# Kernel optimization log

Measured on AMD Instinct MI355X. Metric: run time of the kernel, lower is better.

The kernel has to match this reference:

```python
import jax, jax.numpy as jnp
import numpy as np

FEATURE_DIM = 512
DEPTH = 128
NUM_CLASSES = 1000


def setup_inputs() -> dict:
    key = jax.random.key(0)
    ks = jax.random.split(key, 9)
    s = 1.0 / np.sqrt(FEATURE_DIM)
    sd = 1.0 / np.sqrt(DEPTH)
    return {
        "x": jax.random.normal(ks[0], (8, 2048, FEATURE_DIM), dtype=jnp.float32),
        "Wq": jax.random.uniform(ks[1], (FEATURE_DIM, DEPTH), jnp.float32, -s, s),
        "bq": jax.random.uniform(ks[2], (DEPTH,), jnp.float32, -s, s),
        "Wk": jax.random.uniform(ks[3], (FEATURE_DIM, DEPTH), jnp.float32, -s, s),
        "bk": jax.random.uniform(ks[4], (DEPTH,), jnp.float32, -s, s),
        "Wv": jax.random.uniform(ks[5], (FEATURE_DIM, DEPTH), jnp.float32, -s, s),
        "bv": jax.random.uniform(ks[6], (DEPTH,), jnp.float32, -s, s),
        "Wl": jax.random.uniform(ks[7], (DEPTH, NUM_CLASSES), jnp.float32, -sd, sd),
        "bl": jax.random.uniform(ks[8], (NUM_CLASSES,), jnp.float32, -sd, sd),
    }


def reference(x, Wq, bq, Wk, bk, Wv, bv, Wl, bl):
    # q,k,v: [B,S,depth]
    q = jnp.einsum("bsf,fd->bsd", x, Wq) + bq
    k = jnp.einsum("bsf,fd->bsd", x, Wk) + bk
    v = jnp.einsum("bsf,fd->bsd", x, Wv) + bv
    # NOTE: original applies no 1/sqrt(depth) scaling
    logit = jnp.einsum("bqd,bkd->bqk", q, k)  # [B,S,S]
    attn = jax.nn.softmax(logit, axis=2)
    attn_out = jnp.einsum("bqk,bkd->bqd", attn, v)  # [B,S,depth]
    out = jnp.einsum("bsd,dc->bsc", attn_out, Wl) + bl  # [B,S,C]
    return out.mean(axis=1)  # [B,C]
```

## Files before the change

### kernel.cpp

```cpp
#include <hip/hip_runtime.h>
#include <stdint.h>

#define NB 8
#define SS 2048
#define FF 512
#define DD 128
#define CC 1000
#define KC 8
#define CHUNK (SS / KC)

typedef __attribute__((ext_vector_type(8))) short bf16x8;
typedef __attribute__((ext_vector_type(4))) float f32x4;

__device__ __forceinline__ short f2bf(float f) {
    uint32_t u;
    __builtin_memcpy(&u, &f, 4);
    u = (u + 0x7fffu + ((u >> 16) & 1u)) >> 16;
    return (short)u;
}
__device__ __forceinline__ float bf2f(short h) {
    uint32_t u = ((uint32_t)(uint16_t)h) << 16;
    float f;
    __builtin_memcpy(&f, &u, 4);
    return f;
}
__device__ __forceinline__ void async16(const void* g, void* l) {
    __builtin_amdgcn_global_load_lds(
        (const __attribute__((address_space(1))) uint32_t*)g,
        (__attribute__((address_space(3))) uint32_t*)l, 16, 0, 0);
}

__global__ void prep(const float* __restrict__ x,
                     const float* __restrict__ Wq, const float* __restrict__ Wk,
                     const float* __restrict__ Wv,
                     short* __restrict__ xb, short* __restrict__ Wt)
{
    int bx = blockIdx.x;
    if (bx < 4096) {
        int id = bx * 256 + threadIdx.x;
        const float4* src = (const float4*)x + id * 2;
        float4 a = src[0], b2 = src[1];
        bf16x8 o;
        o[0] = f2bf(a.x);  o[1] = f2bf(a.y);  o[2] = f2bf(a.z);  o[3] = f2bf(a.w);
        o[4] = f2bf(b2.x); o[5] = f2bf(b2.y); o[6] = f2bf(b2.z); o[7] = f2bf(b2.w);
        *(bf16x8*)(xb + id * 8) = o;
    } else {
        int id = (bx - 4096) * 256 + threadIdx.x;
        int w = id >> 16, rem = id & 65535;
        int n = rem >> 9, kx = rem & 511;
        const float* Wsrc = (w == 0) ? Wq : (w == 1) ? Wk : Wv;
        Wt[w * 65536 + n * 512 + kx] = f2bf(Wsrc[kx * 128 + n]);
    }
}

__global__ __launch_bounds__(256) void qkv_proj(
    const short* __restrict__ xb, const short* __restrict__ Wt,
    const float* __restrict__ bq, const float* __restrict__ bk, const float* __restrict__ bv,
    short* __restrict__ qo, short* __restrict__ ko, short* __restrict__ vo)
{
    __shared__ __align__(16) short As[2][128 * 64];
    __shared__ __align__(16) short Bs[2][128 * 64];

    const int m0   = blockIdx.x * 128;
    const int mat  = blockIdx.y;
    const int tid  = threadIdx.x;
    const int wave = tid >> 6, lane = tid & 63;
    const int quad = lane >> 4, l16 = lane & 15;
    const int wr = wave >> 1, wc = wave & 1;

    const short* Wm = Wt + mat * 65536;

    f32x4 acc[4][4];
    for (int i = 0; i < 4; i++)
        for (int j = 0; j < 4; j++) acc[i][j] = (f32x4){0.f, 0.f, 0.f, 0.f};

    const int sr = lane >> 3;
    const int sc = (lane & 7) ^ (sr & 7);

#define QKV_STAGE(buf, kk)                                                  \
    for (int i = 0; i < 4; i++) {                                           \
        int ins = wave * 4 + i;                                             \
        int r = ins * 8 + sr;                                               \
        async16(xb + (m0 + r) * 512 + (kk) + sc * 8, &As[buf][ins * 512]);  \
        async16(Wm + r * 512 + (kk) + sc * 8,        &Bs[buf][ins * 512]);  \
    }

    QKV_STAGE(0, 0)
    __syncthreads();

    int cur = 0;
    for (int t = 0; t < 8; t++) {
        if (t < 7) { QKV_STAGE(cur ^ 1, (t + 1) * 64) }

        for (int kc = 0; kc < 2; kc++) {
            bf16x8 af[4], bfr[4];
            for (int mt = 0; mt < 4; mt++) {
                int R = wr * 64 + mt * 16 + l16, cc = kc * 4 + quad;
                af[mt] = *(const bf16x8*)&As[cur][(R * 8 + (cc ^ (R & 7))) * 8];
            }
            for (int nt = 0; nt < 4; nt++) {
                int R = wc * 64 + nt * 16 + l16, cc = kc * 4 + quad;
                bfr[nt] = *(const bf16x8*)&Bs[cur][(R * 8 + (cc ^ (R & 7))) * 8];
            }
            for (int mt = 0; mt < 4; mt++)
                for (int nt = 0; nt < 4; nt++)
                    acc[mt][nt] = __builtin_amdgcn_mfma_f32_16x16x32_bf16(
                        af[mt], bfr[nt], acc[mt][nt], 0, 0, 0);
        }
        __syncthreads();
        cur ^= 1;
    }
#undef QKV_STAGE

    const float* bias = (mat == 0) ? bq : (mat == 1) ? bk : bv;
    short* outp = (mat == 0) ? qo : (mat == 1) ? ko : vo;
    for (int mt = 0; mt < 4; mt++) {
        int grow_base = m0 + wr * 64 + mt * 16 + quad * 4;
        for (int nt = 0; nt < 4; nt++) {
            int col = wc * 64 + nt * 16 + l16;
            float bb = bias[col];
            for (int r = 0; r < 4; r++)
                outp[(grow_base + r) * 128 + col] = f2bf(acc[mt][nt][r] + bb);
        }
    }
}

__global__ __launch_bounds__(256) void attn_l(
    const short* __restrict__ q, const short* __restrict__ k,
    float* __restrict__ l_part, float* __restrict__ accum)
{
    __shared__ __align__(16) short ks[2][64 * 128];

    const int b  = blockIdx.y;
    const int q0 = blockIdx.x * 128;
    const int lq = blockIdx.z;
    const int c0 = lq * CHUNK;
    const int tid  = threadIdx.x;
    const int wave = tid >> 6, lane = tid & 63;
    const int quad = lane >> 4, l16 = lane & 15;

    if (blockIdx.x == 0 && blockIdx.y == 0 && blockIdx.z == 0) {
        accum[tid] = 0.f; accum[256 + tid] = 0.f;
        accum[512 + tid] = 0.f; accum[768 + tid] = 0.f;
    }

    bf16x8 qf[2][4];
    for (int m = 0; m < 2; m++)
        for (int c = 0; c < 4; c++)
            qf[m][c] = *(const bf16x8*)(q + (b * 2048 + q0 + wave * 32 + m * 16 + l16) * 128
                                          + c * 32 + quad * 8);

    float lsum[2][4] = {{0.f,0.f,0.f,0.f},{0.f,0.f,0.f,0.f}};
    const int krl = lane >> 4;

#define K_STAGE(buf, s0)                                                     \
    for (int i = 0; i < 4; i++) {                                            \
        int ik = wave * 4 + i;                                               \
        int kr = ik * 4 + krl;                                               \
        int kc8 = (lane & 15) ^ (kr & 15);                                   \
        async16(k + (b * 2048 + (s0) + kr) * 128 + kc8 * 8, &ks[buf][ik * 512]); \
    }

    K_STAGE(0, c0)
    __syncthreads();

    int cur = 0;
    for (int t = 0; t < CHUNK / 64; t++) {
        if (t < CHUNK / 64 - 1) { K_STAGE(cur ^ 1, c0 + (t + 1) * 64) }

        for (int ct = 0; ct < 4; ct++) {
            f32x4 Sf[2];
            Sf[0] = (f32x4){0.f,0.f,0.f,0.f};
            Sf[1] = (f32x4){0.f,0.f,0.f,0.f};
            int R = ct * 16 + l16;
            __builtin_amdgcn_s_setprio(1);
            for (int c = 0; c < 4; c++) {
                int cc = c * 4 + quad;
                bf16x8 kb = *(const bf16x8*)&ks[cur][(R * 16 + (cc ^ l16)) * 8];
                for (int m = 0; m < 2; m++)
                    Sf[m] = __builtin_amdgcn_mfma_f32_16x16x32_bf16(
                        qf[m][c], kb, Sf[m], 0, 0, 0);
            }
            __builtin_amdgcn_s_setprio(0);
            for (int m = 0; m < 2; m++)
                for (int r = 0; r < 4; r++)
                    lsum[m][r] += __expf(Sf[m][r] - 10.0f);
        }
        __syncthreads();
        cur ^= 1;
    }

    for (int m = 0; m < 2; m++)
        for (int r = 0; r < 4; r++) {
            float lv = lsum[m][r];
            lv += __shfl_xor(lv, 1);
            lv += __shfl_xor(lv, 2);
            lv += __shfl_xor(lv, 4);
            lv += __shfl_xor(lv, 8);
            if (l16 == 0)
                l_part[(lq * 8 + b) * 2048 + q0 + wave * 32 + m * 16 + quad * 4 + r] = lv;
        }
}

__global__ __launch_bounds__(256) void attn_w(
    const short* __restrict__ q, const short* __restrict__ k,
    const float* __restrict__ l_part, float* __restrict__ w_part)
{
    __shared__ __align__(16) short ks[2][64 * 128];
    __shared__ float wl[4][256];

    const int b  = blockIdx.y;
    const int qt = blockIdx.x;
    const int q0 = qt * 128;
    const int lq = blockIdx.z;
    const int c0 = lq * CHUNK;
    const int tid  = threadIdx.x;
    const int wave = tid >> 6, lane = tid & 63;
    const int quad = lane >> 4, l16 = lane & 15;

    bf16x8 qf[2][4];
    for (int m = 0; m < 2; m++)
        for (int c = 0; c < 4; c++)
            qf[m][c] = *(const bf16x8*)(q + (b * 2048 + q0 + wave * 32 + m * 16 + l16) * 128
                                          + c * 32 + quad * 8);

    float linv[2][4];
    for (int m = 0; m < 2; m++)
        for (int r = 0; r < 4; r++) {
            int row = q0 + wave * 32 + m * 16 + quad * 4 + r;
            float lt = 0.f;
            for (int kc = 0; kc < KC; kc++) lt += l_part[(kc * 8 + b) * 2048 + row];
            linv[m][r] = 1.0f / lt;
        }

    const int krl = lane >> 4;

    K_STAGE(0, c0)
    __syncthreads();

    int cur = 0;
    for (int t = 0; t < CHUNK / 64; t++) {
        if (t < CHUNK / 64 - 1) { K_STAGE(cur ^ 1, c0 + (t + 1) * 64) }
        int s0 = c0 + t * 64;

        for (int ct = 0; ct < 4; ct++) {
            f32x4 Sf[2];
            Sf[0] = (f32x4){0.f,0.f,0.f,0.f};
            Sf[1] = (f32x4){0.f,0.f,0.f,0.f};
            int R = ct * 16 + l16;
            __builtin_amdgcn_s_setprio(1);
            for (int c = 0; c < 4; c++) {
                int cc = c * 4 + quad;
                bf16x8 kb = *(const bf16x8*)&ks[cur][(R * 16 + (cc ^ l16)) * 8];
                for (int m = 0; m < 2; m++)
                    Sf[m] = __builtin_amdgcn_mfma_f32_16x16x32_bf16(
                        qf[m][c], kb, Sf[m], 0, 0, 0);
            }
            __builtin_amdgcn_s_setprio(0);
            float cs = 0.f;
            for (int m = 0; m < 2; m++)
                for (int r = 0; r < 4; r++)
                    cs += __expf(Sf[m][r] - 10.0f) * linv[m][r];
            cs += __shfl_xor(cs, 16);
            cs += __shfl_xor(cs, 32);
            if (quad == 0) wl[wave][(s0 - c0) + ct * 16 + l16] = cs;
        }
        __syncthreads();
        cur ^= 1;
    }
#undef K_STAGE

    {
        float s = wl[0][tid] + wl[1][tid] + wl[2][tid] + wl[3][tid];
        w_part[(qt * 8 + b) * 2048 + c0 + tid] = s;
    }
}

__global__ __launch_bounds__(256) void wv(
    const float* __restrict__ w_part, const short* __restrict__ vo,
    float* __restrict__ accum)
{
    __shared__ float wsh[128];
    __shared__ float red[16][129];
    const int b    = blockIdx.x;
    const int slab = blockIdx.y;
    const int tid  = threadIdx.x;

    if (tid < 128) {
        int s = slab * 128 + tid;
        float wsum = 0.f;
        for (int qt = 0; qt < 16; qt++) wsum += w_part[(qt * 8 + b) * 2048 + s];
        wsh[tid] = wsum;
    }
    __syncthreads();

    const int dgrp = tid & 15, sgrp = tid >> 4;
    const int d0 = dgrp * 8;
    float a[8] = {0.f,0.f,0.f,0.f,0.f,0.f,0.f,0.f};
    for (int i = 0; i < 8; i++) {
        int sl = sgrp * 8 + i;
        bf16x8 v = *(const bf16x8*)(vo + (size_t)(b * 2048 + slab * 128 + sl) * 128 + d0);
        float w = wsh[sl];
        for (int j = 0; j < 8; j++) a[j] += w * bf2f(v[j]);
    }
    for (int j = 0; j < 8; j++) red[sgrp][d0 + j] = a[j];
    __syncthreads();

    if (tid < 128) {
        float s = 0.f;
        for (int g = 0; g < 16; g++) s += red[g][tid];
        atomicAdd(&accum[b * 128 + tid], s);
    }
}

__global__ void final_proj(const float* __restrict__ accum, const float* __restrict__ Wl,
                           const float* __restrict__ bl, float* __restrict__ out)
{
    int id = blockIdx.x * 256 + threadIdx.x;
    if (id >= NB * CC) return;
    int b = id / CC, c = id % CC;
    float s = 0.f;
    for (int d = 0; d < 128; d++)
        s += accum[b * 128 + d] * Wl[d * 1000 + c];
    out[id] = s * (1.0f / 2048.0f) + bl[c];
}

extern "C" void kernel_launch(void* const* d_in, const int* in_sizes, int n_in,
                              void* d_out, int out_size, void* d_ws, size_t ws_size,
                              hipStream_t stream) {
    const float* x  = (const float*)d_in[0];
    const float* Wq = (const float*)d_in[1];
    const float* bq = (const float*)d_in[2];
    const float* Wk = (const float*)d_in[3];
    const float* bk = (const float*)d_in[4];
    const float* Wv = (const float*)d_in[5];
    const float* bv = (const float*)d_in[6];
    const float* Wl = (const float*)d_in[7];
    const float* bl = (const float*)d_in[8];
    float* out = (float*)d_out;

    char* ws = (char*)d_ws;
    short* qo     = (short*)(ws);
    short* ko     = (short*)(ws + 4194304);
    short* vo     = (short*)(ws + 8388608);
    short* xb     = (short*)(ws + 12582912);
    short* Wt     = (short*)(ws + 29360128);
    float* l_part = (float*)(ws + 29753344);
    float* w_part = (float*)(ws + 30277632);
    float* acc    = (float*)(ws + 31326208);

    prep<<<4864, 256, 0, stream>>>(x, Wq, Wk, Wv, xb, Wt);
    qkv_proj<<<dim3(128, 3), 256, 0, stream>>>(xb, Wt, bq, bk, bv, qo, ko, vo);
    attn_l<<<dim3(16, 8, KC), 256, 0, stream>>>(qo, ko, l_part, acc);
    attn_w<<<dim3(16, 8, KC), 256, 0, stream>>>(qo, ko, l_part, w_part);
    wv<<<dim3(8, 16), 256, 0, stream>>>(w_part, vo, acc);
    final_proj<<<(NB * CC + 255) / 256, 256, 0, stream>>>(acc, Wl, bl, out);
}
```

Measured before the change: 148.6 us.

## Store exp scores as bf16 in attn_l and reuse them in attn_wp

In the first attention pass, the exponentiated scores are packed to bf16 and written to a large workspace buffer. A new kernel then reads them back, applies the row normalisation and reduces column weights, so the QK^T MFMA work is not recomputed in a second pass. This replaces recomputation with 64 MB of extra global writes and reads. The buffer overlaps the xb region that prep and qkv_proj no longer need, and it is used only when the workspace is large enough. The stored probabilities are also rounded to bf16, which adds precision loss.

New measurement: 148.8 us. No clear change (+0.1%).

```diff
diff --git a/kernel.cpp b/kernel.cpp
--- a/kernel.cpp
+++ b/kernel.cpp
@@ -11,6 +11,7 @@
 
 typedef __attribute__((ext_vector_type(8))) short bf16x8;
 typedef __attribute__((ext_vector_type(4))) float f32x4;
+typedef __attribute__((ext_vector_type(4))) unsigned int u32x4;
 
 __device__ __forceinline__ short f2bf(float f) {
     uint32_t u;
@@ -23,6 +24,11 @@
     float f;
     __builtin_memcpy(&f, &u, 4);
     return f;
+}
+__device__ __forceinline__ uint32_t cvtpk(float a, float b) {
+    uint32_t r;
+    asm("v_cvt_pk_bf16_f32 %0, %1, %2" : "=v"(r) : "v"(a), "v"(b));
+    return r;
 }
 __device__ __forceinline__ void async16(const void* g, void* l) {
     __builtin_amdgcn_global_load_lds(
@@ -127,19 +133,21 @@
 
 __global__ __launch_bounds__(256) void attn_l(
     const short* __restrict__ q, const short* __restrict__ k,
-    float* __restrict__ l_part, float* __restrict__ accum)
+    float* __restrict__ l_part, float* __restrict__ accum,
+    uint32_t* __restrict__ Pbuf)
 {
     __shared__ __align__(16) short ks[2][64 * 128];
 
     const int b  = blockIdx.y;
-    const int q0 = blockIdx.x * 128;
+    const int qt = blockIdx.x;
+    const int q0 = qt * 128;
     const int lq = blockIdx.z;
     const int c0 = lq * CHUNK;
     const int tid  = threadIdx.x;
     const int wave = tid >> 6, lane = tid & 63;
     const int quad = lane >> 4, l16 = lane & 15;
 
-    if (blockIdx.x == 0 && blockIdx.y == 0 && blockIdx.z == 0) {
+    if (qt == 0 && b == 0 && lq == 0) {
         accum[tid] = 0.f; accum[256 + tid] = 0.f;
         accum[512 + tid] = 0.f; accum[768 + tid] = 0.f;
     }
@@ -152,6 +160,7 @@
 
     float lsum[2][4] = {{0.f,0.f,0.f,0.f},{0.f,0.f,0.f,0.f}};
     const int krl = lane >> 4;
+    const size_t pbase = (size_t)((lq * 8 + b) * 16 + qt) * 16384;
 
 #define K_STAGE(buf, s0)                                                     \
     for (int i = 0; i < 4; i++) {                                            \
@@ -182,9 +191,21 @@
                         qf[m][c], kb, Sf[m], 0, 0, 0);
             }
             __builtin_amdgcn_s_setprio(0);
+            float ev[2][4];
             for (int m = 0; m < 2; m++)
-                for (int r = 0; r < 4; r++)
-                    lsum[m][r] += __expf(Sf[m][r] - 10.0f);
+                for (int r = 0; r < 4; r++) {
+                    ev[m][r] = __expf(Sf[m][r] - 10.0f);
+                    lsum[m][r] += ev[m][r];
+                }
+            if (Pbuf) {
+                u32x4 pk;
+                pk[0] = cvtpk(ev[0][0], ev[0][1]);
+                pk[1] = cvtpk(ev[0][2], ev[0][3]);
+                pk[2] = cvtpk(ev[1][0], ev[1][1]);
+                pk[3] = cvtpk(ev[1][2], ev[1][3]);
+                *(u32x4*)(Pbuf + pbase
+                          + (size_t)((((t * 4 + ct) * 4 + wave) * 64 + lane) * 4)) = pk;
+            }
         }
         __syncthreads();
         cur ^= 1;
@@ -200,6 +221,57 @@
             if (l16 == 0)
                 l_part[(lq * 8 + b) * 2048 + q0 + wave * 32 + m * 16 + quad * 4 + r] = lv;
         }
+}
+
+__global__ __launch_bounds__(256) void attn_wp(
+    const float* __restrict__ l_part, const uint32_t* __restrict__ Pbuf,
+    float* __restrict__ w_part)
+{
+    __shared__ float wl[4][256];
+
+    const int b  = blockIdx.y;
+    const int qt = blockIdx.x;
+    const int q0 = qt * 128;
+    const int lq = blockIdx.z;
+    const int tid  = threadIdx.x;
+    const int wave = tid >> 6, lane = tid & 63;
+    const int quad = lane >> 4, l16 = lane & 15;
+
+    float linv[2][4];
+    for (int m = 0; m < 2; m++)
+        for (int r = 0; r < 4; r++) {
+            int row = q0 + wave * 32 + m * 16 + quad * 4 + r;
+            float lt = 0.f;
+            for (int kc = 0; kc < KC; kc++) lt += l_part[(kc * 8 + b) * 2048 + row];
+            linv[m][r] = 1.0f / lt;
+        }
+
+    const size_t pbase = (size_t)((lq * 8 + b) * 16 + qt) * 16384;
+
+    for (int t = 0; t < CHUNK / 64; t++) {
+        for (int ct = 0; ct < 4; ct++) {
+            u32x4 pk = *(const u32x4*)(Pbuf + pbase
+                        + (size_t)((((t * 4 + ct) * 4 + wave) * 64 + lane) * 4));
+            float cs = 0.f;
+            cs += bf2f((short)(pk[0] & 0xffff)) * linv[0][0];
+            cs += bf2f((short)(pk[0] >> 16))    * linv[0][1];
+            cs += bf2f((short)(pk[1] & 0xffff)) * linv[0][2];
+            cs += bf2f((short)(pk[1] >> 16))    * linv[0][3];
+            cs += bf2f((short)(pk[2] & 0xffff)) * linv[1][0];
+            cs += bf2f((short)(pk[2] >> 16))    * linv[1][1];
+            cs += bf2f((short)(pk[3] & 0xffff)) * linv[1][2];
+            cs += bf2f((short)(pk[3] >> 16))    * linv[1][3];
+            cs += __shfl_xor(cs, 16);
+            cs += __shfl_xor(cs, 32);
+            if (quad == 0) wl[wave][t * 64 + ct * 16 + l16] = cs;
+        }
+    }
+
+    __syncthreads();
+    {
+        float s = wl[0][tid] + wl[1][tid] + wl[2][tid] + wl[3][tid];
+        w_part[(qt * 8 + b) * 2048 + lq * CHUNK + tid] = s;
+    }
 }
 
 __global__ __launch_bounds__(256) void attn_w(
@@ -340,19 +412,39 @@
     float* out = (float*)d_out;
 
     char* ws = (char*)d_ws;
-    short* qo     = (short*)(ws);
-    short* ko     = (short*)(ws + 4194304);
-    short* vo     = (short*)(ws + 8388608);
-    short* xb     = (short*)(ws + 12582912);
-    short* Wt     = (short*)(ws + 29360128);
-    float* l_part = (float*)(ws + 29753344);
-    float* w_part = (float*)(ws + 30277632);
-    float* acc    = (float*)(ws + 31326208);
+    short* qo = (short*)(ws);
+    short* ko = (short*)(ws + 4194304);
+    short* vo = (short*)(ws + 8388608);
+
+    const size_t P_REQ = 81268736ull;
+    bool use_p = ws_size >= P_REQ;
+
+    uint32_t* Pbuf;
+    short *xb, *Wt;
+    float *l_part, *w_part, *acc;
+    if (use_p) {
+        Pbuf   = (uint32_t*)(ws + 12582912);
+        xb     = (short*)(ws + 12582912);
+        Wt     = (short*)(ws + 29360128);
+        l_part = (float*)(ws + 79691776);
+        w_part = (float*)(ws + 80216064);
+        acc    = (float*)(ws + 81264640);
+    } else {
+        Pbuf   = nullptr;
+        xb     = (short*)(ws + 12582912);
+        Wt     = (short*)(ws + 29360128);
+        l_part = (float*)(ws + 29753344);
+        w_part = (float*)(ws + 30277632);
+        acc    = (float*)(ws + 31326208);
+    }
 
     prep<<<4864, 256, 0, stream>>>(x, Wq, Wk, Wv, xb, Wt);
     qkv_proj<<<dim3(128, 3), 256, 0, stream>>>(xb, Wt, bq, bk, bv, qo, ko, vo);
-    attn_l<<<dim3(16, 8, KC), 256, 0, stream>>>(qo, ko, l_part, acc);
-    attn_w<<<dim3(16, 8, KC), 256, 0, stream>>>(qo, ko, l_part, w_part);
+    attn_l<<<dim3(16, 8, KC), 256, 0, stream>>>(qo, ko, l_part, acc, Pbuf);
+    if (use_p)
+        attn_wp<<<dim3(16, 8, KC), 256, 0, stream>>>(l_part, Pbuf, w_part);
+    else
+        attn_w<<<dim3(16, 8, KC), 256, 0, stream>>>(qo, ko, l_part, w_part);
     wv<<<dim3(8, 16), 256, 0, stream>>>(w_part, vo, acc);
     final_proj<<<(NB * CC + 255) / 256, 256, 0, stream>>>(acc, Wl, bl, out);
 }
```

## Fuse attention row-sum and weight passes with grid barrier and register-cached probabilities

Applied to the files above, without the earlier changes.

Merges the two attention kernels into one. The exponentiated scores are kept in registers as packed bf16 and reused after a grid-wide atomic barrier once the row sums are complete, so QK^T no longer has to be recomputed in a second pass. KC drops to 4 so all 512 blocks can be co-resident at two blocks per CU, and q is prescaled by log2(e) so a raw v_exp_f32 replaces __expf. The exchange is high register pressure (128 packed values per thread), bf16 rounding of the probabilities, and a spin barrier that deadlocks if the blocks are not all resident at once.

After: 252.8 us. 70.0% more time.

```diff
diff --git a/kernel.cpp b/kernel.cpp
--- a/kernel.cpp
+++ b/kernel.cpp
@@ -6,8 +6,9 @@
 #define FF 512
 #define DD 128
 #define CC 1000
-#define KC 8
+#define KC 4
 #define CHUNK (SS / KC)
+#define NBLK (16 * 8 * KC)
 
 typedef __attribute__((ext_vector_type(8))) short bf16x8;
 typedef __attribute__((ext_vector_type(4))) float f32x4;
@@ -23,6 +24,16 @@
     float f;
     __builtin_memcpy(&f, &u, 4);
     return f;
+}
+__device__ __forceinline__ uint32_t cvtpk(float a, float b) {
+    uint32_t r;
+    asm("v_cvt_pk_bf16_f32 %0, %1, %2" : "=v"(r) : "v"(a), "v"(b));
+    return r;
+}
+__device__ __forceinline__ float exp2_hw(float x) {
+    float r;
+    asm("v_exp_f32 %0, %1" : "=v"(r) : "v"(x));
+    return r;
 }
 __device__ __forceinline__ void async16(const void* g, void* l) {
     __builtin_amdgcn_global_load_lds(
@@ -56,7 +67,8 @@
 __global__ __launch_bounds__(256) void qkv_proj(
     const short* __restrict__ xb, const short* __restrict__ Wt,
     const float* __restrict__ bq, const float* __restrict__ bk, const float* __restrict__ bv,
-    short* __restrict__ qo, short* __restrict__ ko, short* __restrict__ vo)
+    short* __restrict__ qo, short* __restrict__ ko, short* __restrict__ vo,
+    unsigned int* __restrict__ sem)
 {
     __shared__ __align__(16) short As[2][128 * 64];
     __shared__ __align__(16) short Bs[2][128 * 64];
@@ -68,6 +80,8 @@
     const int quad = lane >> 4, l16 = lane & 15;
     const int wr = wave >> 1, wc = wave & 1;
 
+    if (mat == 0 && blockIdx.x == 0 && tid == 0) *sem = 0u;
+
     const short* Wm = Wt + mat * 65536;
 
     f32x4 acc[4][4];
@@ -114,32 +128,36 @@
 
     const float* bias = (mat == 0) ? bq : (mat == 1) ? bk : bv;
     short* outp = (mat == 0) ? qo : (mat == 1) ? ko : vo;
+    const float scale = (mat == 0) ? 1.44269504f : 1.0f;
     for (int mt = 0; mt < 4; mt++) {
         int grow_base = m0 + wr * 64 + mt * 16 + quad * 4;
         for (int nt = 0; nt < 4; nt++) {
             int col = wc * 64 + nt * 16 + l16;
             float bb = bias[col];
             for (int r = 0; r < 4; r++)
-                outp[(grow_base + r) * 128 + col] = f2bf(acc[mt][nt][r] + bb);
-        }
-    }
-}
-
-__global__ __launch_bounds__(256) void attn_l(
+                outp[(grow_base + r) * 128 + col] = f2bf((acc[mt][nt][r] + bb) * scale);
+        }
+    }
+}
+
+__global__ __launch_bounds__(256, 2) void attn_fused(
     const short* __restrict__ q, const short* __restrict__ k,
-    float* __restrict__ l_part, float* __restrict__ accum)
+    float* __restrict__ l_part, float* __restrict__ w_part,
+    float* __restrict__ accum, unsigned int* __restrict__ sem)
 {
     __shared__ __align__(16) short ks[2][64 * 128];
+    __shared__ float wl[4][512];
 
     const int b  = blockIdx.y;
-    const int q0 = blockIdx.x * 128;
+    const int qt = blockIdx.x;
+    const int q0 = qt * 128;
     const int lq = blockIdx.z;
     const int c0 = lq * CHUNK;
     const int tid  = threadIdx.x;
     const int wave = tid >> 6, lane = tid & 63;
     const int quad = lane >> 4, l16 = lane & 15;
 
-    if (blockIdx.x == 0 && blockIdx.y == 0 && blockIdx.z == 0) {
+    if (qt == 0 && b == 0 && lq == 0) {
         accum[tid] = 0.f; accum[256 + tid] = 0.f;
         accum[512 + tid] = 0.f; accum[768 + tid] = 0.f;
     }
@@ -151,6 +169,7 @@
                                           + c * 32 + quad * 8);
 
     float lsum[2][4] = {{0.f,0.f,0.f,0.f},{0.f,0.f,0.f,0.f}};
+    uint32_t P[8][4][4];
     const int krl = lane >> 4;
 
 #define K_STAGE(buf, s0)                                                     \
@@ -164,33 +183,47 @@
     K_STAGE(0, c0)
     __syncthreads();
 
-    int cur = 0;
-    for (int t = 0; t < CHUNK / 64; t++) {
-        if (t < CHUNK / 64 - 1) { K_STAGE(cur ^ 1, c0 + (t + 1) * 64) }
-
+#pragma unroll
+    for (int t = 0; t < 8; t++) {
+        if (t < 7) { K_STAGE((t + 1) & 1, c0 + (t + 1) * 64) }
+
+#pragma unroll
         for (int ct = 0; ct < 4; ct++) {
             f32x4 Sf[2];
             Sf[0] = (f32x4){0.f,0.f,0.f,0.f};
             Sf[1] = (f32x4){0.f,0.f,0.f,0.f};
             int R = ct * 16 + l16;
             __builtin_amdgcn_s_setprio(1);
+#pragma unroll
             for (int c = 0; c < 4; c++) {
                 int cc = c * 4 + quad;
-                bf16x8 kb = *(const bf16x8*)&ks[cur][(R * 16 + (cc ^ l16)) * 8];
+                bf16x8 kb = *(const bf16x8*)&ks[t & 1][(R * 16 + (cc ^ l16)) * 8];
                 for (int m = 0; m < 2; m++)
                     Sf[m] = __builtin_amdgcn_mfma_f32_16x16x32_bf16(
                         qf[m][c], kb, Sf[m], 0, 0, 0);
             }
             __builtin_amdgcn_s_setprio(0);
+            float e[2][4];
+#pragma unroll
             for (int m = 0; m < 2; m++)
-                for (int r = 0; r < 4; r++)
-                    lsum[m][r] += __expf(Sf[m][r] - 10.0f);
+#pragma unroll
+                for (int r = 0; r < 4; r++) {
+                    e[m][r] = exp2_hw(Sf[m][r] - 14.4269504f);
+                    lsum[m][r] += e[m][r];
+                }
+#pragma unroll
+            for (int m = 0; m < 2; m++) {
+                P[t][ct][m * 2 + 0] = cvtpk(e[m][0], e[m][1]);
+                P[t][ct][m * 2 + 1] = cvtpk(e[m][2], e[m][3]);
+            }
         }
         __syncthreads();
-        cur ^= 1;
-    }
-
+    }
+#undef K_STAGE
+
+#pragma unroll
     for (int m = 0; m < 2; m++)
+#pragma unroll
         for (int r = 0; r < 4; r++) {
             float lv = lsum[m][r];
             lv += __shfl_xor(lv, 1);
@@ -200,79 +233,52 @@
             if (l16 == 0)
                 l_part[(lq * 8 + b) * 2048 + q0 + wave * 32 + m * 16 + quad * 4 + r] = lv;
         }
-}
-
-__global__ __launch_bounds__(256) void attn_w(
-    const short* __restrict__ q, const short* __restrict__ k,
-    const float* __restrict__ l_part, float* __restrict__ w_part)
-{
-    __shared__ __align__(16) short ks[2][64 * 128];
-    __shared__ float wl[4][256];
-
-    const int b  = blockIdx.y;
-    const int qt = blockIdx.x;
-    const int q0 = qt * 128;
-    const int lq = blockIdx.z;
-    const int c0 = lq * CHUNK;
-    const int tid  = threadIdx.x;
-    const int wave = tid >> 6, lane = tid & 63;
-    const int quad = lane >> 4, l16 = lane & 15;
-
-    bf16x8 qf[2][4];
+
+    __threadfence();
+    __syncthreads();
+    if (tid == 0) {
+        __hip_atomic_fetch_add(sem, 1u, __ATOMIC_RELEASE, __HIP_MEMORY_SCOPE_AGENT);
+        while (__hip_atomic_load(sem, __ATOMIC_ACQUIRE, __HIP_MEMORY_SCOPE_AGENT) < NBLK)
+            __builtin_amdgcn_s_sleep(2);
+    }
+    __syncthreads();
+
+    float linv[2][4];
+#pragma unroll
     for (int m = 0; m < 2; m++)
-        for (int c = 0; c < 4; c++)
-            qf[m][c] = *(const bf16x8*)(q + (b * 2048 + q0 + wave * 32 + m * 16 + l16) * 128
-                                          + c * 32 + quad * 8);
-
-    float linv[2][4];
-    for (int m = 0; m < 2; m++)
+#pragma unroll
         for (int r = 0; r < 4; r++) {
             int row = q0 + wave * 32 + m * 16 + quad * 4 + r;
             float lt = 0.f;
-            for (int kc = 0; kc < KC; kc++) lt += l_part[(kc * 8 + b) * 2048 + row];
+            for (int kc = 0; kc < KC; kc++)
+                lt += __hip_atomic_load(&l_part[(kc * 8 + b) * 2048 + row],
+                                        __ATOMIC_RELAXED, __HIP_MEMORY_SCOPE_AGENT);
             linv[m][r] = 1.0f / lt;
         }
 
-    const int krl = lane >> 4;
-
-    K_STAGE(0, c0)
-    __syncthreads();
-
-    int cur = 0;
-    for (int t = 0; t < CHUNK / 64; t++) {
-        if (t < CHUNK / 64 - 1) { K_STAGE(cur ^ 1, c0 + (t + 1) * 64) }
-        int s0 = c0 + t * 64;
-
+#pragma unroll
+    for (int t = 0; t < 8; t++)
+#pragma unroll
         for (int ct = 0; ct < 4; ct++) {
-            f32x4 Sf[2];
-            Sf[0] = (f32x4){0.f,0.f,0.f,0.f};
-            Sf[1] = (f32x4){0.f,0.f,0.f,0.f};
-            int R = ct * 16 + l16;
-            __builtin_amdgcn_s_setprio(1);
-            for (int c = 0; c < 4; c++) {
-                int cc = c * 4 + quad;
-                bf16x8 kb = *(const bf16x8*)&ks[cur][(R * 16 + (cc ^ l16)) * 8];
-                for (int m = 0; m < 2; m++)
-                    Sf[m] = __builtin_amdgcn_mfma_f32_16x16x32_bf16(
-                        qf[m][c], kb, Sf[m], 0, 0, 0);
-            }
-            __builtin_amdgcn_s_setprio(0);
             float cs = 0.f;
-            for (int m = 0; m < 2; m++)
-                for (int r = 0; r < 4; r++)
-                    cs += __expf(Sf[m][r] - 10.0f) * linv[m][r];
+#pragma unroll
+            for (int m = 0; m < 2; m++) {
+                uint32_t u0 = P[t][ct][m * 2 + 0];
+                uint32_t u1 = P[t][ct][m * 2 + 1];
+                cs += bf2f((short)(u0 & 0xffff)) * linv[m][0];
+                cs += bf2f((short)(u0 >> 16))    * linv[m][1];
+                cs += bf2f((short)(u1 & 0xffff)) * linv[m][2];
+                cs += bf2f((short)(u1 >> 16))    * linv[m][3];
+            }
             cs += __shfl_xor(cs, 16);
             cs += __shfl_xor(cs, 32);
-            if (quad == 0) wl[wave][(s0 - c0) + ct * 16 + l16] = cs;
-        }
-        __syncthreads();
-        cur ^= 1;
-    }
-#undef K_STAGE
-
-    {
-        float s = wl[0][tid] + wl[1][tid] + wl[2][tid] + wl[3][tid];
-        w_part[(qt * 8 + b) * 2048 + c0 + tid] = s;
+            if (quad == 0) wl[wave][t * 64 + ct * 16 + l16] = cs;
+        }
+
+    __syncthreads();
+    for (int col = tid; col < 512; col += 256) {
+        float s = wl[0][col] + wl[1][col] + wl[2][col] + wl[3][col];
+        w_part[(qt * 8 + b) * 2048 + c0 + col] = s;
     }
 }
 
@@ -348,11 +354,11 @@
     float* l_part = (float*)(ws + 29753344);
     float* w_part = (float*)(ws + 30277632);
     float* acc    = (float*)(ws + 31326208);
+    unsigned int* sem = (unsigned int*)(ws + 31330304);
 
     prep<<<4864, 256, 0, stream>>>(x, Wq, Wk, Wv, xb, Wt);
-    qkv_proj<<<dim3(128, 3), 256, 0, stream>>>(xb, Wt, bq, bk, bv, qo, ko, vo);
-    attn_l<<<dim3(16, 8, KC), 256, 0, stream>>>(qo, ko, l_part, acc);
-    attn_w<<<dim3(16, 8, KC), 256, 0, stream>>>(qo, ko, l_part, w_part);
+    qkv_proj<<<dim3(128, 3), 256, 0, stream>>>(xb, Wt, bq, bk, bv, qo, ko, vo, sem);
+    attn_fused<<<dim3(16, 8, KC), 256, 0, stream>>>(qo, ko, l_part, w_part, acc, sem);
     wv<<<dim3(8, 16), 256, 0, stream>>>(w_part, vo, acc);
     final_proj<<<(NB * CC + 255) / 256, 256, 0, stream>>>(acc, Wl, bl, out);
 }
```

## Fuse x bf16 conversion into QKV GEMM and fold final projection into wv

Applied to the files above, without the earlier changes.

The separate prep pass that converted x to bf16 is removed. qkv_proj now loads fp32 x into registers, converts it with packed bf16 conversion, and writes it to LDS, with the next tile's loads overlapped with the MFMA work. The final projection kernel is folded into the wv kernel through a last-block-done atomic counter, so the last block computes the output in one pass. This removes the xb round trip to memory and one launch, but it adds register pressure and a serial tail run by a single block.

Measured after the change: 215.6 us. 45.1% more time.

```diff
diff --git a/kernel.cpp b/kernel.cpp
--- a/kernel.cpp
+++ b/kernel.cpp
@@ -11,6 +11,7 @@
 
 typedef __attribute__((ext_vector_type(8))) short bf16x8;
 typedef __attribute__((ext_vector_type(4))) float f32x4;
+typedef __attribute__((ext_vector_type(4))) unsigned int u32x4;
 
 __device__ __forceinline__ short f2bf(float f) {
     uint32_t u;
@@ -24,37 +25,29 @@
     __builtin_memcpy(&f, &u, 4);
     return f;
 }
+__device__ __forceinline__ uint32_t cvtpk(float a, float b) {
+    uint32_t r;
+    asm("v_cvt_pk_bf16_f32 %0, %1, %2" : "=v"(r) : "v"(a), "v"(b));
+    return r;
+}
 __device__ __forceinline__ void async16(const void* g, void* l) {
     __builtin_amdgcn_global_load_lds(
         (const __attribute__((address_space(1))) uint32_t*)g,
         (__attribute__((address_space(3))) uint32_t*)l, 16, 0, 0);
 }
 
-__global__ void prep(const float* __restrict__ x,
-                     const float* __restrict__ Wq, const float* __restrict__ Wk,
-                     const float* __restrict__ Wv,
-                     short* __restrict__ xb, short* __restrict__ Wt)
+__global__ void prep(const float* __restrict__ Wq, const float* __restrict__ Wk,
+                     const float* __restrict__ Wv, short* __restrict__ Wt)
 {
-    int bx = blockIdx.x;
-    if (bx < 4096) {
-        int id = bx * 256 + threadIdx.x;
-        const float4* src = (const float4*)x + id * 2;
-        float4 a = src[0], b2 = src[1];
-        bf16x8 o;
-        o[0] = f2bf(a.x);  o[1] = f2bf(a.y);  o[2] = f2bf(a.z);  o[3] = f2bf(a.w);
-        o[4] = f2bf(b2.x); o[5] = f2bf(b2.y); o[6] = f2bf(b2.z); o[7] = f2bf(b2.w);
-        *(bf16x8*)(xb + id * 8) = o;
-    } else {
-        int id = (bx - 4096) * 256 + threadIdx.x;
-        int w = id >> 16, rem = id & 65535;
-        int n = rem >> 9, kx = rem & 511;
-        const float* Wsrc = (w == 0) ? Wq : (w == 1) ? Wk : Wv;
-        Wt[w * 65536 + n * 512 + kx] = f2bf(Wsrc[kx * 128 + n]);
-    }
+    int id = blockIdx.x * 256 + threadIdx.x;
+    int w = id >> 16, rem = id & 65535;
+    int n = rem >> 9, kx = rem & 511;
+    const float* Wsrc = (w == 0) ? Wq : (w == 1) ? Wk : Wv;
+    Wt[w * 65536 + n * 512 + kx] = f2bf(Wsrc[kx * 128 + n]);
 }
 
 __global__ __launch_bounds__(256) void qkv_proj(
-    const short* __restrict__ xb, const short* __restrict__ Wt,
+    const float* __restrict__ x, const short* __restrict__ Wt,
     const float* __restrict__ bq, const float* __restrict__ bk, const float* __restrict__ bv,
     short* __restrict__ qo, short* __restrict__ ko, short* __restrict__ vo)
 {
@@ -77,20 +70,43 @@
     const int sr = lane >> 3;
     const int sc = (lane & 7) ^ (sr & 7);
 
-#define QKV_STAGE(buf, kk)                                                  \
+    float4 a0[4], a1[4];
+
+#define A_LOAD(kk)                                                          \
     for (int i = 0; i < 4; i++) {                                           \
         int ins = wave * 4 + i;                                             \
         int r = ins * 8 + sr;                                               \
-        async16(xb + (m0 + r) * 512 + (kk) + sc * 8, &As[buf][ins * 512]);  \
-        async16(Wm + r * 512 + (kk) + sc * 8,        &Bs[buf][ins * 512]);  \
-    }
-
-    QKV_STAGE(0, 0)
+        const float4* s4 = (const float4*)(x + (size_t)(m0 + r) * 512 + (kk) + sc * 8); \
+        a0[i] = s4[0]; a1[i] = s4[1];                                       \
+    }
+#define A_WRITE(buf)                                                        \
+    for (int i = 0; i < 4; i++) {                                           \
+        int ins = wave * 4 + i;                                             \
+        u32x4 p;                                                            \
+        p[0] = cvtpk(a0[i].x, a0[i].y);                                     \
+        p[1] = cvtpk(a0[i].z, a0[i].w);                                     \
+        p[2] = cvtpk(a1[i].x, a1[i].y);                                     \
+        p[3] = cvtpk(a1[i].z, a1[i].w);                                     \
+        *(u32x4*)&As[buf][ins * 512 + lane * 8] = p;                        \
+    }
+#define B_STAGE(buf, kk)                                                    \
+    for (int i = 0; i < 4; i++) {                                           \
+        int ins = wave * 4 + i;                                             \
+        int r = ins * 8 + sr;                                               \
+        async16(Wm + r * 512 + (kk) + sc * 8, &Bs[buf][ins * 512]);         \
+    }
+
+    A_LOAD(0)
+    B_STAGE(0, 0)
+    A_WRITE(0)
     __syncthreads();
 
     int cur = 0;
     for (int t = 0; t < 8; t++) {
-        if (t < 7) { QKV_STAGE(cur ^ 1, (t + 1) * 64) }
+        if (t < 7) {
+            A_LOAD((t + 1) * 64)
+            B_STAGE(cur ^ 1, (t + 1) * 64)
+        }
 
         for (int kc = 0; kc < 2; kc++) {
             bf16x8 af[4], bfr[4];
@@ -107,10 +123,13 @@
                     acc[mt][nt] = __builtin_amdgcn_mfma_f32_16x16x32_bf16(
                         af[mt], bfr[nt], acc[mt][nt], 0, 0, 0);
         }
+        if (t < 7) { A_WRITE(cur ^ 1) }
         __syncthreads();
         cur ^= 1;
     }
-#undef QKV_STAGE
+#undef A_LOAD
+#undef A_WRITE
+#undef B_STAGE
 
     const float* bias = (mat == 0) ? bq : (mat == 1) ? bk : bv;
     short* outp = (mat == 0) ? qo : (mat == 1) ? ko : vo;
@@ -127,7 +146,8 @@
 
 __global__ __launch_bounds__(256) void attn_l(
     const short* __restrict__ q, const short* __restrict__ k,
-    float* __restrict__ l_part, float* __restrict__ accum)
+    float* __restrict__ l_part, float* __restrict__ accum,
+    unsigned int* __restrict__ cnt)
 {
     __shared__ __align__(16) short ks[2][64 * 128];
 
@@ -142,6 +162,7 @@
     if (blockIdx.x == 0 && blockIdx.y == 0 && blockIdx.z == 0) {
         accum[tid] = 0.f; accum[256 + tid] = 0.f;
         accum[512 + tid] = 0.f; accum[768 + tid] = 0.f;
+        if (tid == 0) *cnt = 0u;
     }
 
     bf16x8 qf[2][4];
@@ -276,12 +297,16 @@
     }
 }
 
-__global__ __launch_bounds__(256) void wv(
+__global__ __launch_bounds__(256) void wv_final(
     const float* __restrict__ w_part, const short* __restrict__ vo,
-    float* __restrict__ accum)
+    float* __restrict__ accum, const float* __restrict__ Wl,
+    const float* __restrict__ bl, float* __restrict__ out,
+    unsigned int* __restrict__ cnt)
 {
-    __shared__ float wsh[128];
-    __shared__ float red[16][129];
+    __shared__ float smem[9024];
+    __shared__ unsigned int lastflag;
+    float* wsh = smem;
+    float (*red)[129] = (float (*)[129])(smem + 128);
     const int b    = blockIdx.x;
     const int slab = blockIdx.y;
     const int tid  = threadIdx.x;
@@ -311,18 +336,50 @@
         for (int g = 0; g < 16; g++) s += red[g][tid];
         atomicAdd(&accum[b * 128 + tid], s);
     }
-}
-
-__global__ void final_proj(const float* __restrict__ accum, const float* __restrict__ Wl,
-                           const float* __restrict__ bl, float* __restrict__ out)
-{
-    int id = blockIdx.x * 256 + threadIdx.x;
-    if (id >= NB * CC) return;
-    int b = id / CC, c = id % CC;
-    float s = 0.f;
-    for (int d = 0; d < 128; d++)
-        s += accum[b * 128 + d] * Wl[d * 1000 + c];
-    out[id] = s * (1.0f / 2048.0f) + bl[c];
+
+    __threadfence();
+    __syncthreads();
+    if (tid == 0)
+        lastflag = (__hip_atomic_fetch_add(cnt, 1u, __ATOMIC_ACQ_REL,
+                        __HIP_MEMORY_SCOPE_AGENT) == 127u) ? 1u : 0u;
+    __syncthreads();
+    if (lastflag == 0u) return;
+
+    float* acc_l = smem;
+    float* wlb   = smem + 1024;
+    for (int i = tid; i < 1024; i += 256)
+        acc_l[i] = __hip_atomic_load(&accum[i], __ATOMIC_RELAXED,
+                                     __HIP_MEMORY_SCOPE_AGENT);
+    __syncthreads();
+
+    float o[4][8];
+    for (int j = 0; j < 4; j++)
+        for (int bb = 0; bb < 8; bb++) o[j][bb] = 0.f;
+
+    for (int dc = 0; dc < 128; dc += 8) {
+        for (int i = tid; i < 8000; i += 256)
+            wlb[i] = Wl[(dc + i / 1000) * 1000 + (i % 1000)];
+        __syncthreads();
+        for (int j = 0; j < 4; j++) {
+            int c = tid + j * 256;
+            if (c < 1000)
+                for (int dd = 0; dd < 8; dd++) {
+                    float wv_ = wlb[dd * 1000 + c];
+                    for (int bb = 0; bb < 8; bb++)
+                        o[j][bb] += acc_l[bb * 128 + dc + dd] * wv_;
+                }
+        }
+        __syncthreads();
+    }
+
+    for (int j = 0; j < 4; j++) {
+        int c = tid + j * 256;
+        if (c < 1000) {
+            float blc = bl[c];
+            for (int bb = 0; bb < 8; bb++)
+                out[bb * 1000 + c] = o[j][bb] * (1.0f / 2048.0f) + blc;
+        }
+    }
 }
 
 extern "C" void kernel_launch(void* const* d_in, const int* in_sizes, int n_in,
@@ -343,16 +400,15 @@
     short* qo     = (short*)(ws);
     short* ko     = (short*)(ws + 4194304);
     short* vo     = (short*)(ws + 8388608);
-    short* xb     = (short*)(ws + 12582912);
-    short* Wt     = (short*)(ws + 29360128);
-    float* l_part = (float*)(ws + 29753344);
-    float* w_part = (float*)(ws + 30277632);
-    float* acc    = (float*)(ws + 31326208);
-
-    prep<<<4864, 256, 0, stream>>>(x, Wq, Wk, Wv, xb, Wt);
-    qkv_proj<<<dim3(128, 3), 256, 0, stream>>>(xb, Wt, bq, bk, bv, qo, ko, vo);
-    attn_l<<<dim3(16, 8, KC), 256, 0, stream>>>(qo, ko, l_part, acc);
+    short* Wt     = (short*)(ws + 12582912);
+    float* l_part = (float*)(ws + 12976128);
+    float* w_part = (float*)(ws + 13500416);
+    float* acc    = (float*)(ws + 14548992);
+    unsigned int* cnt = (unsigned int*)(ws + 14553088);
+
+    prep<<<768, 256, 0, stream>>>(Wq, Wk, Wv, Wt);
+    qkv_proj<<<dim3(128, 3), 256, 0, stream>>>(x, Wt, bq, bk, bv, qo, ko, vo);
+    attn_l<<<dim3(16, 8, KC), 256, 0, stream>>>(qo, ko, l_part, acc, cnt);
     attn_w<<<dim3(16, 8, KC), 256, 0, stream>>>(qo, ko, l_part, w_part);
-    wv<<<dim3(8, 16), 256, 0, stream>>>(w_part, vo, acc);
-    final_proj<<<(NB * CC + 255) / 256, 256, 0, stream>>>(acc, Wl, bl, out);
-}
+    wv_final<<<dim3(8, 16), 256, 0, stream>>>(w_part, vo, acc, Wl, bl, out, cnt);
+}
```
